# Kernel tuning notes

Measured on AMD Instinct MI355X. Metric: run time of the kernel, lower is better.

The kernel has to match this reference:

```python
import jax, jax.numpy as jnp
import numpy as np

HIST, CNTX, PRED = 336, 168, 24
C = 1            # c_in == c_out == 1 (univariate)
HID = 128        # GRU hidden size
NFEAT = 5        # hourly time features (freq_map['H'])
EMB = 10 * NFEAT # embedding_dim * freq_map['H'] = 50
NLAGS = HIST - CNTX            # 168 lag taps
IN_DIM = EMB + NLAGS           # rnn input size = 218
NSAMP = 8192     # num_parallel_samples


def setup_inputs() -> dict:
    key = jax.random.key(0)
    ks = jax.random.split(key, 8)
    s = lambda fan: 1.0 / np.sqrt(fan)
    return {
        "x": jax.random.normal(ks[0], (1, HIST, C), jnp.float32),
        "x_mark": jax.random.normal(ks[1], (1, HIST, NFEAT), jnp.float32),
        "y_mark": jax.random.normal(ks[2], (1, PRED, NFEAT), jnp.float32),
        "W_emb": jax.random.normal(ks[3], (NFEAT, EMB), jnp.float32) * s(NFEAT),
        "b_emb": jnp.zeros((EMB,), jnp.float32),
        "W_ih": jax.random.normal(ks[4], (3 * HID, IN_DIM), jnp.float32) * s(IN_DIM),
        "W_hh": jax.random.normal(ks[5], (3 * HID, HID), jnp.float32) * s(HID),
        "b_ih": jnp.zeros((3 * HID,), jnp.float32),
        "b_hh": jnp.zeros((3 * HID,), jnp.float32),
        "W_proj": jax.random.normal(ks[6], (HID, 3), jnp.float32) * s(HID),
        "b_proj": jnp.zeros((3,), jnp.float32),
        "mode": 0,
    }


def reference(x, x_mark, y_mark, W_emb, b_emb, W_ih, W_hh, b_ih, b_hh, W_proj, b_proj, mode):

    def gru_step(h, xt):  # PyTorch GRU cell semantics (gate order r,z,n)
        gi = xt @ W_ih.T + b_ih
        gh = h @ W_hh.T + b_hh
        i_r, i_z, i_n = jnp.split(gi, 3, axis=-1)
        h_r, h_z, h_n = jnp.split(gh, 3, axis=-1)
        r = jax.nn.sigmoid(i_r + h_r)
        z = jax.nn.sigmoid(i_z + h_z)
        n = jnp.tanh(i_n + r * h_n)
        return (1.0 - z) * n + z * h

    B = x.shape[0]  # 1
    # ----- unroll_encoder (y=None path) -----
    # mean_abs_scaling over last cntx_len steps
    scale = jnp.clip(jnp.mean(jnp.abs(x[:, -CNTX:, :]), axis=1, keepdims=True), 1e-5, None)  # (B,1,C)
    xs = x / scale  # scaled sequence (lags/scale == lags of scaled sequence)
    # lagged subsequences: lag indices 1..NLAGS, subsequence length CNTX
    t_idx = (HIST - CNTX) + jnp.arange(CNTX)[:, None] - jnp.arange(1, NLAGS + 1)[None, :]  # (CNTX, NLAGS)
    lags = xs[:, t_idx, 0]  # (B, CNTX, NLAGS)  (C==1 so flatten is trivial)
    tf = x_mark[:, HIST - CNTX:, :] @ W_emb + b_emb  # (B, CNTX, EMB)
    enc_in = jnp.concatenate([lags, tf], axis=-1)  # (B, CNTX, IN_DIM)
    h0 = jnp.zeros((B, HID), x.dtype)
    h_last, _ = jax.lax.scan(lambda h, xt: (gru_step(h, xt), None), h0,
                             jnp.swapaxes(enc_in, 0, 1))  # final GRU state (B,HID)

    # ----- sampling_decoder -----
    sc = scale[0, 0, 0]  # scalar (B=1, C=1)
    h = jnp.broadcast_to(h_last, (NSAMP, HID))                       # repeat state over samples
    ym = jnp.broadcast_to(y_mark @ W_emb + b_emb, (NSAMP, PRED, EMB))  # repeated embedded marks
    buf = jnp.broadcast_to(x[0, -NLAGS:, 0], (NSAMP, NLAGS))         # last NLAGS observed values
    key0 = jax.random.key(42)

    def step(carry, ym_k):
        buf, h, key = carry
        key, sk = jax.random.split(key)
        lag_in = buf[:, ::-1] / sc                 # decoder lags: most recent first
        xin = jnp.concatenate([lag_in, ym_k], axis=-1)  # (S, IN_DIM)
        h = gru_step(h, xin)
        p = h @ W_proj + b_proj                    # (S, 3) StudentT arg projection
        df = 2.0 + jax.nn.softplus(p[:, 0])
        loc = p[:, 1]
        sigma = jax.nn.softplus(p[:, 2])
        t = jax.random.t(sk, df, shape=df.shape)
        samp = (loc + sigma * t) * sc              # affine-transformed StudentT sample
        buf = jnp.concatenate([buf[:, 1:], samp[:, None]], axis=1)
        return (buf, h, key), samp

    _, samples = jax.lax.scan(step, (buf, h, key0), jnp.swapaxes(ym, 0, 1))  # (PRED, S)
    return samples.T[:, :, None]  # (num_parallel_samples, pred_len, c_out)
```

## Files before the change

kernel.cpp:

```cpp
#include <hip/hip_runtime.h>
#include <stdint.h>

#define HIST 336
#define CNTX 168
#define PRED 24
#define HID 128
#define NFEAT 5
#define EMB 50
#define NLAGS 168
#define IN_DIM 218
#define NSAMP 8192
#define G3 384

#define WS_XS     0
#define WS_SC     336
#define WS_TF     340
#define WS_YM     8740
#define WS_KEYS   9940
#define WS_ENCGI  10036
#define WS_WQ     10036
#define WS_GISH   74548
#define WS_HLAST  83764
#define WS_WIHT   83892

typedef float v2f __attribute__((ext_vector_type(2)));
__device__ __forceinline__ v2f fma2(v2f a, v2f b, v2f c){ return __builtin_elementwise_fma(a,b,c); }

__device__ __forceinline__ uint32_t rotl32(uint32_t v, int r){ return (v<<r)|(v>>(32-r)); }

__device__ __forceinline__ void threefry(uint32_t k0, uint32_t k1, uint32_t x0, uint32_t x1,
                                         uint32_t &o0, uint32_t &o1){
  uint32_t ks2 = k0 ^ k1 ^ 0x1BD11BDAu;
  x0 += k0; x1 += k1;
#define TFR(a) { x0 += x1; x1 = rotl32(x1,(a)); x1 ^= x0; }
  TFR(13) TFR(15) TFR(26) TFR(6)
  x0 += k1; x1 += ks2 + 1u;
  TFR(17) TFR(29) TFR(16) TFR(24)
  x0 += ks2; x1 += k0 + 2u;
  TFR(13) TFR(15) TFR(26) TFR(6)
  x0 += k0; x1 += k1 + 3u;
  TFR(17) TFR(29) TFR(16) TFR(24)
  x0 += k1; x1 += ks2 + 4u;
  TFR(13) TFR(15) TFR(26) TFR(6)
  x0 += ks2; x1 += k0 + 5u;
#undef TFR
  o0 = x0; o1 = x1;
}

__device__ __forceinline__ void tf_split2(uint32_t k0, uint32_t k1,
                                          uint32_t &a0, uint32_t &a1,
                                          uint32_t &b0, uint32_t &b1){
  threefry(k0,k1, 0u,0u, a0,a1);
  threefry(k0,k1, 0u,1u, b0,b1);
}

__device__ __forceinline__ void tf_split3(uint32_t k0, uint32_t k1,
                                          uint32_t &a0, uint32_t &a1,
                                          uint32_t &b0, uint32_t &b1,
                                          uint32_t &c0, uint32_t &c1){
  threefry(k0,k1, 0u,0u, a0,a1);
  threefry(k0,k1, 0u,1u, b0,b1);
  threefry(k0,k1, 0u,2u, c0,c1);
}

__device__ __forceinline__ uint32_t tf_bits1(uint32_t k0, uint32_t k1){
  uint32_t o0,o1; threefry(k0,k1, 0u,0u, o0,o1); return o0 ^ o1;
}

__device__ __forceinline__ uint32_t tf_bits_at(uint32_t k0, uint32_t k1, uint32_t i){
  uint32_t o0,o1; threefry(k0,k1, 0u,i, o0,o1); return o0 ^ o1;
}

__device__ __forceinline__ float bits_to_f01(uint32_t b){
  return __uint_as_float((b>>9) | 0x3f800000u) - 1.0f;
}

__device__ __forceinline__ float erfinv32(float x){
  float w = -log1pf(-x*x);
  float p;
  if (w < 5.0f){
    w = w - 2.5f;
    p = 2.81022636e-08f;
    p = fmaf(p, w, 3.43273939e-07f);
    p = fmaf(p, w, -3.5233877e-06f);
    p = fmaf(p, w, -4.39150654e-06f);
    p = fmaf(p, w, 0.00021858087f);
    p = fmaf(p, w, -0.00125372503f);
    p = fmaf(p, w, -0.00417768164f);
    p = fmaf(p, w, 0.246640727f);
    p = fmaf(p, w, 1.50140941f);
  } else {
    w = sqrtf(w) - 3.0f;
    p = -0.000200214257f;
    p = fmaf(p, w, 0.000100950558f);
    p = fmaf(p, w, 0.00134934322f);
    p = fmaf(p, w, -0.00367342844f);
    p = fmaf(p, w, 0.00573950773f);
    p = fmaf(p, w, -0.0076224613f);
    p = fmaf(p, w, 0.00943887047f);
    p = fmaf(p, w, 1.00167406f);
    p = fmaf(p, w, 2.83297682f);
  }
  return p*x;
}

__device__ __forceinline__ float normal_from_key(uint32_t k0, uint32_t k1){
  uint32_t b = tf_bits1(k0,k1);
  const float lo = -0.99999994f;
  float f = bits_to_f01(b);
  float u = fmaxf(lo, f*2.0f + lo);
  return 1.41421356f * erfinv32(u);
}

__device__ float gamma_sample(uint32_t k0, uint32_t k1, float alpha){
  float d = __fsub_rn(alpha, 0.33333334f);
  float c = 0.33333334f / sqrtf(d);
  uint32_t ck0,ck1, sb0,sb1;
  tf_split2(k0,k1, ck0,ck1, sb0,sb1);
  float V;
  for(;;){
    uint32_t nk0,nk1, xk0,xk1, uk0,uk1;
    tf_split3(ck0,ck1, nk0,nk1, xk0,xk1, uk0,uk1);
    ck0=nk0; ck1=nk1;
    float x, v;
    do {
      uint32_t xa0,xa1, xb0,xb1;
      tf_split2(xk0,xk1, xa0,xa1, xb0,xb1);
      xk0=xa0; xk1=xa1;
      x = normal_from_key(xb0,xb1);
      v = __fadd_rn(1.0f, __fmul_rn(x, c));
    } while (v <= 0.0f);
    float X  = __fmul_rn(x, x);
    float Vv = __fmul_rn(__fmul_rn(v, v), v);
    float U  = bits_to_f01(tf_bits1(uk0,uk1));
    float t1 = __fsub_rn(1.0f, __fmul_rn(0.0331f, __fmul_rn(X, X)));
    bool cont = (U >= t1);
    if (cont){
      float lhs = logf(U);
      float rhs = __fadd_rn(__fmul_rn(0.5f, X),
                  __fmul_rn(d, __fadd_rn(__fsub_rn(1.0f, Vv), logf(Vv))));
      cont = (lhs >= rhs);
    }
    if (!cont){ V = Vv; break; }
  }
  return d*V;
}

__device__ __forceinline__ float softplus_f(float x){
  float amax = fmaxf(x, 0.0f);
  return amax + log1pf(expf(-fabsf(x)));
}

__global__ __launch_bounds__(256) void k1_prep(const float* __restrict__ x,
                                               const float* __restrict__ xmark,
                                               const float* __restrict__ ymark,
                                               const float* __restrict__ Wemb,
                                               const float* __restrict__ bemb,
                                               float* __restrict__ ws){
  __shared__ float red[256];
  __shared__ float s_sc;
  int t = threadIdx.x;
  float a = 0.f;
  if (t < CNTX) a = fabsf(x[CNTX + t]);
  red[t] = a;
  __syncthreads();
  for(int s=128; s>0; s>>=1){ if(t<s) red[t]+=red[t+s]; __syncthreads(); }
  if (t==0){ s_sc = fmaxf(red[0]/168.0f, 1e-5f); ws[WS_SC]=s_sc; }
  __syncthreads();
  float sc = s_sc;
  for(int i=t; i<HIST; i+=256) ws[WS_XS+i] = x[i]/sc;
  for(int idx=t; idx<CNTX*EMB; idx+=256){
    int tt = idx/EMB, e = idx%EMB;
    float acc = bemb[e];
    for(int f=0; f<NFEAT; f++) acc += xmark[(CNTX+tt)*NFEAT+f]*Wemb[f*EMB+e];
    ws[WS_TF+idx] = acc;
  }
  for(int idx=t; idx<PRED*EMB; idx+=256){
    int kk = idx/EMB, e = idx%EMB;
    float acc = bemb[e];
    for(int f=0; f<NFEAT; f++) acc += ymark[kk*NFEAT+f]*Wemb[f*EMB+e];
    ws[WS_YM+idx] = acc;
  }
  if (t==0){
    uint32_t* kp = reinterpret_cast<uint32_t*>(ws + WS_KEYS);
    uint32_t c0 = 0u, c1 = 42u;
    for(int k=0;k<PRED;k++){
      uint32_t a0,a1,b0,b1;
      tf_split2(c0,c1, a0,a1, b0,b1);
      c0=a0; c1=a1;
      uint32_t n0,n1,g0,g1;
      tf_split2(b0,b1, n0,n1, g0,g1);
      kp[k*4+0]=n0; kp[k*4+1]=n1; kp[k*4+2]=g0; kp[k*4+3]=g1;
    }
  }
}

__global__ __launch_bounds__(256) void k2_gi(const float* __restrict__ Wih,
                                             const float* __restrict__ bih,
                                             const float* __restrict__ bhh,
                                             float* __restrict__ ws){
  int idx = blockIdx.x*256 + threadIdx.x;
  if (idx < G3*192){
    int r = idx / 192, t = idx % 192;
    const float* wr = Wih + r*IN_DIM;
    const float* xs = ws + WS_XS;
    float acc = bih[r] + (r < 256 ? bhh[r] : 0.0f);
    if (t < CNTX){
      const float* tf = ws + WS_TF + t*EMB;
      for(int j=0;j<NLAGS;j++) acc += wr[j]*xs[CNTX + t - 1 - j];
      for(int e=0;e<EMB;e++)   acc += wr[NLAGS+e]*tf[e];
      ws[WS_ENCGI + t*G3 + r] = acc;
    } else {
      int k = t - CNTX;
      const float* ym = ws + WS_YM + k*EMB;
      for(int e=0;e<EMB;e++)   acc += wr[NLAGS+e]*ym[e];
      for(int i=k;i<NLAGS;i++) acc += wr[i]*xs[HIST-1-i+k];
      ws[WS_GISH + k*G3 + r] = acc;
    }
  } else {
    int j = idx - G3*192;
    if (j < PRED*G3){
      int r = j / PRED, i = j % PRED;
      ws[WS_WIHT + i*G3 + r] = Wih[r*IN_DIM + i];
    }
  }
}

__global__ __launch_bounds__(384) void k3_enc(const float* __restrict__ Whh,
                                              const float* __restrict__ bhh,
                                              float* __restrict__ ws){
  __shared__ __align__(16) float h[HID];
  __shared__ float grz[256];
  __shared__ float hnv[HID];
  int r = threadIdx.x;
  float4 w[32];
  const float4* wr = (const float4*)(Whh + r*HID);
  #pragma unroll
  for(int i=0;i<32;i++) w[i] = wr[i];
  float bh = (r>=256)? bhh[r] : 0.0f;
  if (r < HID) h[r] = 0.0f;
  __syncthreads();
  const float* encgi = ws + WS_ENCGI;
  for(int t=0;t<CNTX;t++){
    float acc = 0.f;
    #pragma unroll
    for(int i=0;i<32;i++){
      float4 hv = *(const float4*)&h[4*i];
      float4 ww = w[i];
      acc = fmaf(ww.x,hv.x, fmaf(ww.y,hv.y, fmaf(ww.z,hv.z, fmaf(ww.w,hv.w, acc))));
    }
    if (r < 256) grz[r] = encgi[t*G3+r] + acc;
    else         hnv[r-256] = acc + bh;
    __syncthreads();
    if (r < HID){
      float rr = 1.0f/(1.0f+expf(-grz[r]));
      float zz = 1.0f/(1.0f+expf(-grz[128+r]));
      float inv = encgi[t*G3+256+r];
      float nn = tanhf(inv + rr*hnv[r]);
      h[r] = (1.0f-zz)*nn + zz*h[r];
    }
    __syncthreads();
  }
  if (r < HID) ws[WS_HLAST + r] = h[r];
  float4* wq = (float4*)(ws + WS_WQ);
  for(int idx=r; idx<32*G3; idx+=384){
    int q = idx / G3, rr = idx % G3;
    wq[idx] = *(const float4*)&Whh[rr*HID + q*4];
  }
}

#define SPB 32
#define THR4 512

__global__ __launch_bounds__(512) void k4_dec(const float* __restrict__ Whh,
                                              const float* __restrict__ bhh,
                                              const float* __restrict__ Wproj,
                                              const float* __restrict__ bproj,
                                              const float* __restrict__ ws,
                                              float* __restrict__ out){
  __shared__ __align__(16) float4 hT4[128][9];
  __shared__ float wihT_l[24*G3];
  __shared__ float shistT[25][34];
  __shared__ float parr[SPB][4];
  __shared__ float wp[HID*3];
  __shared__ float bp[3];
  __shared__ uint32_t skeys[PRED*4];

  int t = threadIdx.x;
  int b = blockIdx.x;
  int rg = t & 127;
  int sg = t >> 7;
  int s0 = sg*8;
  int g0 = sg*2;

  float bhn = bhh[256 + rg];

  for(int idx=t; idx<24*G3; idx+=THR4) wihT_l[idx] = ws[WS_WIHT + idx];
  for(int idx=t; idx<HID*3; idx+=THR4) wp[idx] = Wproj[idx];
  if (t < 3) bp[t] = bproj[t];
  if (t < PRED*4) skeys[t] = reinterpret_cast<const uint32_t*>(ws + WS_KEYS)[t];
  if (t < 128){
    float hl = ws[WS_HLAST + t];
    float4 v = {hl,hl,hl,hl};
    #pragma unroll
    for(int g=0;g<8;g++) hT4[t][g] = v;
  }
  float hold[8];
  {
    float hl = ws[WS_HLAST + rg];
    #pragma unroll
    for(int s=0;s<8;s++) hold[s] = hl;
  }
  float sc = ws[WS_SC];
  const float* gish = ws + WS_GISH;
  const float4* Wq4 = (const float4*)(ws + WS_WQ);
  __syncthreads();

  #pragma unroll 1
  for(int k=0;k<PRED;k++){
    v2f aR[4], aZ[4], aH[4], aI[4];
    {
      float gR = gish[k*G3 + rg];
      float gZ = gish[k*G3 + 128 + rg];
      float gI = gish[k*G3 + 256 + rg];
      #pragma unroll
      for(int p=0;p<4;p++){
        aR[p] = (v2f){gR,gR}; aZ[p] = (v2f){gZ,gZ};
        aI[p] = (v2f){gI,gI}; aH[p] = (v2f){bhn,bhn};
      }
    }
    #pragma unroll 1
    for(int i=0;i<k;i++){
      float wR = wihT_l[i*G3 + rg];
      float wZ = wihT_l[i*G3 + 128 + rg];
      float wN = wihT_l[i*G3 + 256 + rg];
      v2f wR2 = {wR,wR}, wZ2 = {wZ,wZ}, wN2 = {wN,wN};
      #pragma unroll
      for(int p=0;p<4;p++){
        v2f sh = *(const v2f*)&shistT[k-1-i][s0 + 2*p];
        aR[p] = fma2(wR2, sh, aR[p]);
        aZ[p] = fma2(wZ2, sh, aZ[p]);
        aI[p] = fma2(wN2, sh, aI[p]);
      }
    }
    #pragma unroll 1
    for(int q=0;q<32;q++){
      float4 wr4 = Wq4[q*G3 + rg];
      float4 wz4 = Wq4[q*G3 + 128 + rg];
      float4 wn4 = Wq4[q*G3 + 256 + rg];
      #pragma unroll
      for(int c=0;c<4;c++){
        float wrc = (c==0)?wr4.x:(c==1)?wr4.y:(c==2)?wr4.z:wr4.w;
        float wzc = (c==0)?wz4.x:(c==1)?wz4.y:(c==2)?wz4.z:wz4.w;
        float wnc = (c==0)?wn4.x:(c==1)?wn4.y:(c==2)?wn4.z:wn4.w;
        v2f wr2 = {wrc,wrc}, wz2 = {wzc,wzc}, wn2 = {wnc,wnc};
        #pragma unroll
        for(int g=0;g<2;g++){
          float4 hv = hT4[4*q + c][g0 + g];
          v2f lo = {hv.x, hv.y}, hi = {hv.z, hv.w};
          aR[2*g]   = fma2(wr2, lo, aR[2*g]);
          aR[2*g+1] = fma2(wr2, hi, aR[2*g+1]);
          aZ[2*g]   = fma2(wz2, lo, aZ[2*g]);
          aZ[2*g+1] = fma2(wz2, hi, aZ[2*g+1]);
          aH[2*g]   = fma2(wn2, lo, aH[2*g]);
          aH[2*g+1] = fma2(wn2, hi, aH[2*g+1]);
        }
      }
    }
    __syncthreads();
    #pragma unroll
    for(int s=0;s<8;s++){
      int p = s >> 1, e = s & 1;
      float aRv = aR[p][e], aZv = aZ[p][e], aIv = aI[p][e], aHv = aH[p][e];
      float rr = 1.0f/(1.0f+expf(-aRv));
      float zz = 1.0f/(1.0f+expf(-aZv));
      float nn = tanhf(aIv + rr*aHv);
      float hn = (1.0f-zz)*nn + zz*hold[s];
      hold[s] = hn;
      ((float*)&hT4[rg][g0 + (s>>2)])[s & 3] = hn;
    }
    __syncthreads();
    if (t < SPB*3){
      int s = t/3, c2 = t%3;
      const float* hT = (const float*)hT4;
      float acc = bp[c2];
      for(int l=0;l<HID;l++) acc = fmaf(hT[l*36 + s], wp[l*3+c2], acc);
      parr[s][c2] = acc;
    }
    __syncthreads();
    if (t < SPB){
      int s = t, gs = b*SPB + s;
      float p0 = parr[s][0], loc = parr[s][1], p2 = parr[s][2];
      float df = 2.0f + softplus_f(p0);
      float half_df = df*0.5f;
      float sigma = softplus_f(p2);
      uint32_t kn0 = skeys[k*4+0], kn1 = skeys[k*4+1];
      uint32_t kg0 = skeys[k*4+2], kg1 = skeys[k*4+3];
      uint32_t bnb = tf_bits_at(kn0, kn1, (uint32_t)gs);
      const float lo = -0.99999994f;
      float un = fmaxf(lo, bits_to_f01(bnb)*2.0f + lo);
      float nval = 1.41421356f * erfinv32(un);
      uint32_t gk0, gk1;
      threefry(kg0, kg1, 0u, (uint32_t)gs, gk0, gk1);
      float gmm = gamma_sample(gk0, gk1, half_df);
      float tval = nval * sqrtf(half_df / gmm);
      float samp = (loc + sigma*tval)*sc;
      out[gs*PRED + k] = samp;
      shistT[k][s] = samp / sc;
    }
    __syncthreads();
  }
}

extern "C" void kernel_launch(void* const* d_in, const int* in_sizes, int n_in,
                              void* d_out, int out_size, void* d_ws, size_t ws_size,
                              hipStream_t stream){
  const float* x     = (const float*)d_in[0];
  const float* xmark = (const float*)d_in[1];
  const float* ymark = (const float*)d_in[2];
  const float* Wemb  = (const float*)d_in[3];
  const float* bemb  = (const float*)d_in[4];
  const float* Wih   = (const float*)d_in[5];
  const float* Whh   = (const float*)d_in[6];
  const float* bih   = (const float*)d_in[7];
  const float* bhh   = (const float*)d_in[8];
  const float* Wproj = (const float*)d_in[9];
  const float* bproj = (const float*)d_in[10];
  float* ws  = (float*)d_ws;
  float* out = (float*)d_out;

  hipLaunchKernelGGL(k1_prep, dim3(1), dim3(256), 0, stream, x, xmark, ymark, Wemb, bemb, ws);
  hipLaunchKernelGGL(k2_gi, dim3((G3*192 + PRED*G3 + 255)/256), dim3(256), 0, stream, Wih, bih, bhh, ws);
  hipLaunchKernelGGL(k3_enc, dim3(1), dim3(384), 0, stream, Whh, bhh, ws);
  hipLaunchKernelGGL(k4_dec, dim3(NSAMP/SPB), dim3(THR4), 0, stream, Whh, bhh, Wproj, bproj, ws, out);
}
```

Baseline: 712.7 us.

## Precompute df-independent RNG draws for all steps before the decoder loop

The normal draw, first gamma-rejection candidate and uniform, and follow-on keys do not depend on the df value from the network. They are now computed for all 24 steps up front, spread across all 512 threads, and stored in shared memory. The serial per-step tail, which ran on only 32 threads, then only does the df-dependent acceptance test and falls back to the full rejection loop when needed. The projection pass is also folded into that tail, removing one barrier. The cost is a larger shared-memory footprint, which may reduce occupancy.

```diff
diff --git a/kernel.cpp b/kernel.cpp
--- a/kernel.cpp
+++ b/kernel.cpp
@@ -112,40 +112,6 @@
   return 1.41421356f * erfinv32(u);
 }
 
-__device__ float gamma_sample(uint32_t k0, uint32_t k1, float alpha){
-  float d = __fsub_rn(alpha, 0.33333334f);
-  float c = 0.33333334f / sqrtf(d);
-  uint32_t ck0,ck1, sb0,sb1;
-  tf_split2(k0,k1, ck0,ck1, sb0,sb1);
-  float V;
-  for(;;){
-    uint32_t nk0,nk1, xk0,xk1, uk0,uk1;
-    tf_split3(ck0,ck1, nk0,nk1, xk0,xk1, uk0,uk1);
-    ck0=nk0; ck1=nk1;
-    float x, v;
-    do {
-      uint32_t xa0,xa1, xb0,xb1;
-      tf_split2(xk0,xk1, xa0,xa1, xb0,xb1);
-      xk0=xa0; xk1=xa1;
-      x = normal_from_key(xb0,xb1);
-      v = __fadd_rn(1.0f, __fmul_rn(x, c));
-    } while (v <= 0.0f);
-    float X  = __fmul_rn(x, x);
-    float Vv = __fmul_rn(__fmul_rn(v, v), v);
-    float U  = bits_to_f01(tf_bits1(uk0,uk1));
-    float t1 = __fsub_rn(1.0f, __fmul_rn(0.0331f, __fmul_rn(X, X)));
-    bool cont = (U >= t1);
-    if (cont){
-      float lhs = logf(U);
-      float rhs = __fadd_rn(__fmul_rn(0.5f, X),
-                  __fmul_rn(d, __fadd_rn(__fsub_rn(1.0f, Vv), logf(Vv))));
-      cont = (lhs >= rhs);
-    }
-    if (!cont){ V = Vv; break; }
-  }
-  return d*V;
-}
-
 __device__ __forceinline__ float softplus_f(float x){
   float amax = fmaxf(x, 0.0f);
   return amax + log1pf(expf(-fabsf(x)));
@@ -281,10 +247,14 @@
   __shared__ __align__(16) float4 hT4[128][9];
   __shared__ float wihT_l[24*G3];
   __shared__ float shistT[25][34];
-  __shared__ float parr[SPB][4];
   __shared__ float wp[HID*3];
   __shared__ float bp[3];
   __shared__ uint32_t skeys[PRED*4];
+  __shared__ float nv[PRED][SPB];
+  __shared__ float gx1[PRED][SPB];
+  __shared__ float gU1[PRED][SPB];
+  __shared__ uint32_t gnk[PRED][SPB][2];
+  __shared__ uint32_t gxa[PRED][SPB][2];
 
   int t = threadIdx.x;
   int b = blockIdx.x;
@@ -314,6 +284,29 @@
   float sc = ws[WS_SC];
   const float* gish = ws + WS_GISH;
   const float4* Wq4 = (const float4*)(ws + WS_WQ);
+  __syncthreads();
+
+  for(int idx=t; idx<PRED*SPB; idx+=THR4){
+    int kk = idx >> 5, s = idx & 31;
+    uint32_t gs = (uint32_t)(b*SPB + s);
+    uint32_t kn0 = skeys[kk*4+0], kn1 = skeys[kk*4+1];
+    uint32_t kg0 = skeys[kk*4+2], kg1 = skeys[kk*4+3];
+    uint32_t bnb = tf_bits_at(kn0, kn1, gs);
+    const float lo = -0.99999994f;
+    float un = fmaxf(lo, bits_to_f01(bnb)*2.0f + lo);
+    nv[kk][s] = 1.41421356f * erfinv32(un);
+    uint32_t gk0,gk1; threefry(kg0, kg1, 0u, gs, gk0, gk1);
+    uint32_t ck0,ck1, sb0,sb1;
+    tf_split2(gk0,gk1, ck0,ck1, sb0,sb1);
+    uint32_t nk0,nk1, xk0,xk1, uk0,uk1;
+    tf_split3(ck0,ck1, nk0,nk1, xk0,xk1, uk0,uk1);
+    uint32_t xa0,xa1, xb0,xb1;
+    tf_split2(xk0,xk1, xa0,xa1, xb0,xb1);
+    gx1[kk][s] = normal_from_key(xb0,xb1);
+    gU1[kk][s] = bits_to_f01(tf_bits1(uk0,uk1));
+    gnk[kk][s][0]=nk0; gnk[kk][s][1]=nk1;
+    gxa[kk][s][0]=xa0; gxa[kk][s][1]=xa1;
+  }
   __syncthreads();
 
   #pragma unroll 1
@@ -380,29 +373,78 @@
       ((float*)&hT4[rg][g0 + (s>>2)])[s & 3] = hn;
     }
     __syncthreads();
-    if (t < SPB*3){
-      int s = t/3, c2 = t%3;
-      const float* hT = (const float*)hT4;
-      float acc = bp[c2];
-      for(int l=0;l<HID;l++) acc = fmaf(hT[l*36 + s], wp[l*3+c2], acc);
-      parr[s][c2] = acc;
-    }
-    __syncthreads();
     if (t < SPB){
       int s = t, gs = b*SPB + s;
-      float p0 = parr[s][0], loc = parr[s][1], p2 = parr[s][2];
+      const float* hT = (const float*)hT4;
+      float p0 = bp[0], p1 = bp[1], p2 = bp[2];
+      for(int l=0;l<HID;l++){
+        float hv = hT[l*36 + s];
+        p0 = fmaf(hv, wp[l*3+0], p0);
+        p1 = fmaf(hv, wp[l*3+1], p1);
+        p2 = fmaf(hv, wp[l*3+2], p2);
+      }
+      float loc = p1;
       float df = 2.0f + softplus_f(p0);
       float half_df = df*0.5f;
       float sigma = softplus_f(p2);
-      uint32_t kn0 = skeys[k*4+0], kn1 = skeys[k*4+1];
-      uint32_t kg0 = skeys[k*4+2], kg1 = skeys[k*4+3];
-      uint32_t bnb = tf_bits_at(kn0, kn1, (uint32_t)gs);
-      const float lo = -0.99999994f;
-      float un = fmaxf(lo, bits_to_f01(bnb)*2.0f + lo);
-      float nval = 1.41421356f * erfinv32(un);
-      uint32_t gk0, gk1;
-      threefry(kg0, kg1, 0u, (uint32_t)gs, gk0, gk1);
-      float gmm = gamma_sample(gk0, gk1, half_df);
+      float d_ = __fsub_rn(half_df, 0.33333334f);
+      float c_ = 0.33333334f / sqrtf(d_);
+      float x = gx1[k][s];
+      float U = gU1[k][s];
+      uint32_t xk0 = gxa[k][s][0], xk1 = gxa[k][s][1];
+      uint32_t ck0 = gnk[k][s][0], ck1 = gnk[k][s][1];
+      float v = __fadd_rn(1.0f, __fmul_rn(x, c_));
+      while (v <= 0.0f){
+        uint32_t xa0,xa1, xb0,xb1;
+        tf_split2(xk0,xk1, xa0,xa1, xb0,xb1);
+        xk0=xa0; xk1=xa1;
+        x = normal_from_key(xb0,xb1);
+        v = __fadd_rn(1.0f, __fmul_rn(x, c_));
+      }
+      float V; bool done = false;
+      {
+        float X  = __fmul_rn(x, x);
+        float Vv = __fmul_rn(__fmul_rn(v, v), v);
+        float t1 = __fsub_rn(1.0f, __fmul_rn(0.0331f, __fmul_rn(X, X)));
+        bool cont = (U >= t1);
+        if (cont){
+          float lhs = logf(U);
+          float rhs = __fadd_rn(__fmul_rn(0.5f, X),
+                      __fmul_rn(d_, __fadd_rn(__fsub_rn(1.0f, Vv), logf(Vv))));
+          cont = (lhs >= rhs);
+        }
+        if (!cont){ V = Vv; done = true; }
+      }
+      if (!done){
+        for(;;){
+          uint32_t nk0,nk1, xkb0,xkb1, uk0,uk1;
+          tf_split3(ck0,ck1, nk0,nk1, xkb0,xkb1, uk0,uk1);
+          ck0=nk0; ck1=nk1;
+          float xx, vv;
+          uint32_t xc0 = xkb0, xc1 = xkb1;
+          do {
+            uint32_t xa0,xa1, xb0,xb1;
+            tf_split2(xc0,xc1, xa0,xa1, xb0,xb1);
+            xc0=xa0; xc1=xa1;
+            xx = normal_from_key(xb0,xb1);
+            vv = __fadd_rn(1.0f, __fmul_rn(xx, c_));
+          } while (vv <= 0.0f);
+          float X  = __fmul_rn(xx, xx);
+          float Vv = __fmul_rn(__fmul_rn(vv, vv), vv);
+          float Uu = bits_to_f01(tf_bits1(uk0,uk1));
+          float t1 = __fsub_rn(1.0f, __fmul_rn(0.0331f, __fmul_rn(X, X)));
+          bool cont = (Uu >= t1);
+          if (cont){
+            float lhs = logf(Uu);
+            float rhs = __fadd_rn(__fmul_rn(0.5f, X),
+                        __fmul_rn(d_, __fadd_rn(__fsub_rn(1.0f, Vv), logf(Vv))));
+            cont = (lhs >= rhs);
+          }
+          if (!cont){ V = Vv; break; }
+        }
+      }
+      float gmm = d_*V;
+      float nval = nv[k][s];
       float tval = nval * sqrtf(half_df / gmm);
       float samp = (loc + sigma*tval)*sc;
       out[gs*PRED + k] = samp;
```

Result: no change. 712.9 us (+0.0%).
